# Performance work log

Measured on AMD Instinct MI355X. Metric: run time of the kernel, lower is better.

The kernel has to match this reference:

```python
import jax, jax.numpy as jnp
import numpy as np

D = 256       # hp.encoder_dim
F = 256       # hp.duration_predictor_filter_size
K = 3         # hp.duration_predictor_kernel_size
ALPHA = 1.0
EPS = 1e-5


def _conv1d(x, w):
    # x: [N, L, Cin], w: [K, Cin, Cout], 'same' padding=1 for K=3
    return jax.lax.conv_general_dilated(
        x, w, window_strides=(1,), padding=((1, 1),),
        dimension_numbers=('NWC', 'WIO', 'NWC'))


def _layer_norm(h, g, b):
    mu = jnp.mean(h, axis=-1, keepdims=True)
    var = jnp.var(h, axis=-1, keepdims=True)
    return (h - mu) * jax.lax.rsqrt(var + EPS) * g + b


def setup_inputs() -> dict:
    key = jax.random.key(0)
    ks = jax.random.split(key, 12)
    N, L = 16, 512
    xavier_cw = float(np.sqrt(2.0 / (D * K + F * K)))  # xavier-ish for conv
    xavier_lw = float(np.sqrt(2.0 / (F + 1)))
    return {
        'x': jax.random.normal(ks[0], (N, L, D), dtype=jnp.float32),
        'conv1_w': jax.random.normal(ks[1], (K, D, F), dtype=jnp.float32) * xavier_cw,
        'conv1_b': jnp.zeros((F,), dtype=jnp.float32),
        'ln1_g': jnp.ones((F,), dtype=jnp.float32),
        'ln1_b': jnp.zeros((F,), dtype=jnp.float32),
        'conv2_w': jax.random.normal(ks[2], (K, F, F), dtype=jnp.float32) * xavier_cw,
        'conv2_b': jnp.zeros((F,), dtype=jnp.float32),
        'ln2_g': jnp.ones((F,), dtype=jnp.float32),
        'ln2_b': jnp.zeros((F,), dtype=jnp.float32),
        'lin_w': jax.random.normal(ks[3], (F, 1), dtype=jnp.float32) * xavier_lw,
        'lin_b': jnp.zeros((1,), dtype=jnp.float32),
        'WVF_max_length': 4096,
    }


def reference(x, conv1_w, conv1_b, ln1_g, ln1_b, conv2_w, conv2_b,
              ln2_g, ln2_b, lin_w, lin_b, WVF_max_length):
    # ---- DurationPredictor (eval mode: dropout = identity) ----
    h = _conv1d(x, conv1_w) + conv1_b            # [N, L, F]
    h = jax.nn.relu(_layer_norm(h, ln1_g, ln1_b))
    h = _conv1d(h, conv2_w) + conv2_b
    h = jax.nn.relu(_layer_norm(h, ln2_g, ln2_b))
    dpo = jax.nn.relu(h @ lin_w + lin_b)[..., 0]  # [N, L]

    # ---- LengthRegulator (no attn): int durations, alignment @ x ----
    dur = ((dpo + 0.5) * ALPHA).astype(jnp.int32)  # [N, L]
    ends = jnp.cumsum(dur, axis=-1)                # inclusive cumsum
    starts = ends - dur                            # exclusive cumsum
    t = jnp.arange(WVF_max_length)                 # static output length
    # alignment[n, t, l] = 1 iff starts[n,l] <= t < ends[n,l]
    align = ((t[None, :, None] >= starts[:, None, :]) &
             (t[None, :, None] < ends[:, None, :])).astype(x.dtype)  # [N, T, L]
    out = jnp.einsum('ntl,nld->ntd', align, x)     # [N, T, D]

    WVF_pos = jnp.arange(1, WVF_max_length + 1, dtype=jnp.int64
                         if jax.config.jax_enable_x64 else jnp.int32)[None, :]
    return out, WVF_pos
```

## Files before the change

kernel.cpp:

```cpp
#include <hip/hip_runtime.h>
#include <hip/hip_fp8.h>
#include <math.h>

#define N_   16
#define L_   512
#define C_   256
#define T_   4096
#define EPSL 1e-5f
#define BM   32

typedef float f32x4 __attribute__((ext_vector_type(4)));

__device__ __forceinline__ unsigned char f2q(float f) {
    __hip_fp8_e4m3 q(f);
    return (unsigned char)q.__x;
}

__global__ __launch_bounds__(256) void pack_w_kernel(
    const float* __restrict__ w1, const float* __restrict__ w2,
    unsigned char* __restrict__ bpk1, unsigned char* __restrict__ bpk2,
    float* __restrict__ wpos)
{
    int gid = blockIdx.x * 256 + threadIdx.x;
    if (gid < T_) wpos[gid] = (float)(gid + 1);
    const float* w      = (gid < 24576) ? w1 : w2;
    unsigned char* bpk  = (gid < 24576) ? bpk1 : bpk2;
    int g2 = gid & 24575;
    int lane = g2 & 63;
    int s    = (g2 >> 6) & 7;
    int cg   = (g2 >> 9) & 15;
    int karm = g2 >> 13;
    int cin0 = s * 32 + (lane >> 4) * 8;
    int cout = cg * 16 + (lane & 15);
    const float* src = w + (size_t)(karm * 256 + cin0) * 256 + cout;
    unsigned long long o = 0;
    #pragma unroll
    for (int e = 0; e < 8; ++e)
        o |= (unsigned long long)f2q(src[(size_t)e * 256]) << (8 * e);
    *reinterpret_cast<unsigned long long*>(bpk + (size_t)g2 * 8) = o;
}

#define LDB(BPK, KARM, DST) do {                                              \
    const unsigned char* bb_ = (BPK) + ((size_t)((KARM) * 16 + cg0)) * 4096 + lane * 8; \
    _Pragma("unroll")                                                         \
    for (int s_ = 0; s_ < 8; ++s_) {                                          \
        DST[s_]     = *reinterpret_cast<const long*>(bb_ + s_ * 512);         \
        DST[8 + s_] = *reinterpret_cast<const long*>(bb_ + 4096 + s_ * 512);  \
    } } while (0)

#define AOFF(BUF, RA, S)                                                      \
    (BUF + (RA) * 256 + (((((S) << 1) + (lg >> 1)) ^ ((RA) & 15)) << 4) + ((lg & 1) << 3))

#define CONV1K(KARM, B) do {                                                  \
    _Pragma("unroll")                                                         \
    for (int s_ = 0; s_ < 8; ++s_) {                                          \
        _Pragma("unroll")                                                     \
        for (int t_ = 0; t_ < 3; ++t_) {                                      \
            int rA_ = 16 * t_ + lr + (KARM);                                  \
            long a_ = *reinterpret_cast<const long*>(AOFF(xt, rA_, s_));      \
            acc1[t_][0] = __builtin_amdgcn_mfma_f32_16x16x32_fp8_fp8(a_, B[s_],     acc1[t_][0], 0, 0, 0); \
            acc1[t_][1] = __builtin_amdgcn_mfma_f32_16x16x32_fp8_fp8(a_, B[8 + s_], acc1[t_][1], 0, 0, 0); \
        } } } while (0)

#define CONV2K(KARM, B) do {                                                  \
    _Pragma("unroll")                                                         \
    for (int s_ = 0; s_ < 8; ++s_) {                                          \
        _Pragma("unroll")                                                     \
        for (int t_ = 0; t_ < 2; ++t_) {                                      \
            int rA_ = 16 * t_ + lr + (KARM);                                  \
            long a_ = *reinterpret_cast<const long*>(AOFF(h1t, rA_, s_));     \
            c2[t_][0] = __builtin_amdgcn_mfma_f32_16x16x32_fp8_fp8(a_, B[s_],     c2[t_][0], 0, 0, 0); \
            c2[t_][1] = __builtin_amdgcn_mfma_f32_16x16x32_fp8_fp8(a_, B[8 + s_], c2[t_][1], 0, 0, 0); \
        } } } while (0)

__global__ __launch_bounds__(512) void fused_conv_kernel(
    const float* __restrict__ x,
    const unsigned char* __restrict__ bpk1, const unsigned char* __restrict__ bpk2,
    const float* __restrict__ b1, const float* __restrict__ g1, const float* __restrict__ be1,
    const float* __restrict__ b2, const float* __restrict__ g2, const float* __restrict__ be2,
    const float* __restrict__ lw, const float* __restrict__ lb,
    int* __restrict__ dur)
{
    __shared__ __align__(16) char xt[50 * 256];
    __shared__ __align__(16) char h1t[34 * 256];
    __shared__ float redS[8][48], redQ[8][48], redP[8][32];

    const int tid  = threadIdx.x;
    const int wv   = tid >> 6;
    const int lane = tid & 63;
    const int lg   = lane >> 4;
    const int lr   = lane & 15;
    const int n    = blockIdx.x >> 4;
    const int l0   = (blockIdx.x & 15) << 5;
    const int cg0  = wv * 2;
    const int col0 = wv * 32 + lr, col1 = col0 + 16;

    long Ba[16], Bb[16];
    LDB(bpk1, 0, Ba);

    for (int idx = tid; idx < 36 * 16; idx += 512) {
        int r = idx >> 4, slot = idx & 15;
        int l = l0 - 2 + r;
        unsigned int pk[4] = {0, 0, 0, 0};
        if (l >= 0 && l < L_) {
            const float* src = x + (((size_t)(n * L_ + l)) << 8) + (slot << 4);
            #pragma unroll
            for (int q = 0; q < 4; ++q) {
                f32x4 f = *reinterpret_cast<const f32x4*>(src + q * 4);
                pk[q] = (unsigned int)f2q(f[0]) | ((unsigned int)f2q(f[1]) << 8) |
                        ((unsigned int)f2q(f[2]) << 16) | ((unsigned int)f2q(f[3]) << 24);
            }
        }
        *reinterpret_cast<uint4*>(xt + r * 256 + ((slot ^ (r & 15)) << 4)) =
            make_uint4(pk[0], pk[1], pk[2], pk[3]);
    }
    __syncthreads();

    f32x4 acc1[3][2] = {};
    LDB(bpk1, 1, Bb);  CONV1K(0, Ba);
    LDB(bpk1, 2, Ba);  CONV1K(1, Bb);
    LDB(bpk2, 0, Bb);  CONV1K(2, Ba);
    LDB(bpk2, 1, Ba);

    const float cb10 = b1[col0], cb11 = b1[col1];
    const float cg10 = g1[col0], cg11 = g1[col1];
    const float ce10 = be1[col0], ce11 = be1[col1];
    {
        float sv[12], qv[12];
        #pragma unroll
        for (int t = 0; t < 3; ++t)
            #pragma unroll
            for (int j = 0; j < 4; ++j) {
                float h0 = acc1[t][0][j] + cb10, h1 = acc1[t][1][j] + cb11;
                sv[t*4+j] = h0 + h1; qv[t*4+j] = h0 * h0 + h1 * h1;
            }
        #pragma unroll
        for (int m = 1; m < 16; m <<= 1)
            #pragma unroll
            for (int k = 0; k < 12; ++k) {
                sv[k] += __shfl_xor(sv[k], m, 64);
                qv[k] += __shfl_xor(qv[k], m, 64);
            }
        if (lr == 0) {
            #pragma unroll
            for (int t = 0; t < 3; ++t)
                #pragma unroll
                for (int j = 0; j < 4; ++j) {
                    redS[wv][16*t + lg*4 + j] = sv[t*4+j];
                    redQ[wv][16*t + lg*4 + j] = qv[t*4+j];
                }
        }
    }
    __syncthreads();
    if (tid < 48) {
        float ss = 0.f, qq = 0.f;
        #pragma unroll
        for (int u = 0; u < 8; ++u) { ss += redS[u][tid]; qq += redQ[u][tid]; }
        float m_  = ss * (1.f / 256.f);
        float var = fmaxf(qq * (1.f / 256.f) - m_ * m_, 0.f);
        redS[0][tid] = m_;
        redQ[0][tid] = 1.0f / sqrtf(var + EPSL);
    }
    __syncthreads();

    #pragma unroll
    for (int t = 0; t < 3; ++t)
        #pragma unroll
        for (int j = 0; j < 4; ++j) {
            int hr = 16*t + lg*4 + j;
            if (hr < 34) {
                int hl = l0 - 1 + hr;
                float r0 = 0.f, r1 = 0.f;
                if (hl >= 0 && hl < L_) {
                    r0 = fmaxf((acc1[t][0][j] + cb10 - redS[0][hr]) * redQ[0][hr] * cg10 + ce10, 0.f);
                    r1 = fmaxf((acc1[t][1][j] + cb11 - redS[0][hr]) * redQ[0][hr] * cg11 + ce11, 0.f);
                }
                *(unsigned char*)(h1t + hr*256 + (((col0 >> 4) ^ (hr & 15)) << 4) + (col0 & 15)) = f2q(r0);
                *(unsigned char*)(h1t + hr*256 + (((col1 >> 4) ^ (hr & 15)) << 4) + (col1 & 15)) = f2q(r1);
            }
        }
    __syncthreads();

    f32x4 c2[2][2] = {};
    CONV2K(0, Bb);  LDB(bpk2, 2, Bb);
    CONV2K(1, Ba);
    CONV2K(2, Bb);

    const float cb20 = b2[col0], cb21 = b2[col1];
    const float cg20 = g2[col0], cg21 = g2[col1];
    const float ce20 = be2[col0], ce21 = be2[col1];
    const float lw0  = lw[col0],  lw1  = lw[col1];
    {
        float sv[8], qv[8];
        #pragma unroll
        for (int tt = 0; tt < 2; ++tt)
            #pragma unroll
            for (int j = 0; j < 4; ++j) {
                float h0 = c2[tt][0][j] + cb20, h1 = c2[tt][1][j] + cb21;
                sv[tt*4+j] = h0 + h1; qv[tt*4+j] = h0 * h0 + h1 * h1;
            }
        #pragma unroll
        for (int m = 1; m < 16; m <<= 1)
            #pragma unroll
            for (int k = 0; k < 8; ++k) {
                sv[k] += __shfl_xor(sv[k], m, 64);
                qv[k] += __shfl_xor(qv[k], m, 64);
            }
        if (lr == 0) {
            #pragma unroll
            for (int tt = 0; tt < 2; ++tt)
                #pragma unroll
                for (int j = 0; j < 4; ++j) {
                    redS[wv][16*tt + lg*4 + j] = sv[tt*4+j];
                    redQ[wv][16*tt + lg*4 + j] = qv[tt*4+j];
                }
        }
    }
    __syncthreads();
    if (tid < 32) {
        float ss = 0.f, qq = 0.f;
        #pragma unroll
        for (int u = 0; u < 8; ++u) { ss += redS[u][tid]; qq += redQ[u][tid]; }
        float m_  = ss * (1.f / 256.f);
        float var = fmaxf(qq * (1.f / 256.f) - m_ * m_, 0.f);
        redS[0][tid] = m_;
        redQ[0][tid] = 1.0f / sqrtf(var + EPSL);
    }
    __syncthreads();

    {
        float pv[8];
        #pragma unroll
        for (int tt = 0; tt < 2; ++tt)
            #pragma unroll
            for (int j = 0; j < 4; ++j) {
                int r = 16*tt + lg*4 + j;
                float r0 = fmaxf((c2[tt][0][j] + cb20 - redS[0][r]) * redQ[0][r] * cg20 + ce20, 0.f);
                float r1 = fmaxf((c2[tt][1][j] + cb21 - redS[0][r]) * redQ[0][r] * cg21 + ce21, 0.f);
                pv[tt*4+j] = r0 * lw0 + r1 * lw1;
            }
        #pragma unroll
        for (int m = 1; m < 16; m <<= 1)
            #pragma unroll
            for (int k = 0; k < 8; ++k)
                pv[k] += __shfl_xor(pv[k], m, 64);
        if (lr == 0) {
            #pragma unroll
            for (int tt = 0; tt < 2; ++tt)
                #pragma unroll
                for (int j = 0; j < 4; ++j)
                    redP[wv][16*tt + lg*4 + j] = pv[tt*4+j];
        }
    }
    __syncthreads();
    if (tid < 32) {
        float dot = lb[0];
        #pragma unroll
        for (int u = 0; u < 8; ++u) dot += redP[u][tid];
        dur[n * L_ + l0 + tid] = (int)(fmaxf(dot, 0.f) + 0.5f);
    }
}

__global__ __launch_bounds__(512) void gather_kernel(
    const float* __restrict__ x, const int* __restrict__ dur,
    float* __restrict__ out)
{
    __shared__ __align__(16) int se[L_];
    const int wid = threadIdx.x >> 6, lane = threadIdx.x & 63;
    const int blk = blockIdx.x;
    const int n = blk >> 9;

    if (wid == 0) {
        const int* dsrc = dur + n * L_;
        int4 va = reinterpret_cast<const int4*>(dsrc)[lane * 2];
        int4 vb = reinterpret_cast<const int4*>(dsrc)[lane * 2 + 1];
        int p0 = va.x,      p1 = p0 + va.y, p2 = p1 + va.z, p3 = p2 + va.w;
        int p4 = p3 + vb.x, p5 = p4 + vb.y, p6 = p5 + vb.z, p7 = p6 + vb.w;
        int tot = p7;
        #pragma unroll
        for (int m = 1; m < 64; m <<= 1) {
            int tu = __shfl_up(tot, m, 64);
            if (lane >= m) tot += tu;
        }
        int off = tot - p7;
        reinterpret_cast<int4*>(se)[lane * 2]     = make_int4(p0+off, p1+off, p2+off, p3+off);
        reinterpret_cast<int4*>(se)[lane * 2 + 1] = make_int4(p4+off, p5+off, p6+off, p7+off);
    }
    __syncthreads();

    const int t = ((blk & 511) << 3) + wid;
    const int total = se[L_ - 1];

    f32x4 v = {0.f, 0.f, 0.f, 0.f};
    if (t < total) {
        int p = 0;
        #pragma unroll
        for (int step = 256; step > 0; step >>= 1)
            if (p + step <= L_ && se[p + step - 1] <= t) p += step;
        v = reinterpret_cast<const f32x4*>(x + (((size_t)(n * L_ + p)) << 8))[lane];
    }
    __builtin_nontemporal_store(
        v, reinterpret_cast<f32x4*>(out + (((size_t)(n * T_ + t)) << 8)) + lane);
}

extern "C" void kernel_launch(void* const* d_in, const int* in_sizes, int n_in,
                              void* d_out, int out_size, void* d_ws, size_t ws_size,
                              hipStream_t stream)
{
    const float* x   = (const float*)d_in[0];
    const float* w1  = (const float*)d_in[1];
    const float* b1  = (const float*)d_in[2];
    const float* g1  = (const float*)d_in[3];
    const float* be1 = (const float*)d_in[4];
    const float* w2  = (const float*)d_in[5];
    const float* b2  = (const float*)d_in[6];
    const float* g2  = (const float*)d_in[7];
    const float* be2 = (const float*)d_in[8];
    const float* lw  = (const float*)d_in[9];
    const float* lb  = (const float*)d_in[10];

    float* out = (float*)d_out;
    unsigned char* bpk1 = (unsigned char*)d_out;
    unsigned char* bpk2 = bpk1 + 196608;
    int* dur = (int*)d_ws;

    pack_w_kernel<<<192, 256, 0, stream>>>(w1, w2, bpk1, bpk2,
                                           out + (size_t)N_ * T_ * C_);

    fused_conv_kernel<<<N_ * (L_ / BM), 512, 0, stream>>>(
        x, bpk1, bpk2, b1, g1, be1, b2, g2, be2, lw, lb, dur);

    gather_kernel<<<N_ * T_ / 8, 512, 0, stream>>>(x, dur, out);
}
```

Before: 37.25 us.

## Halve conv row tile to 16 and use 4 waves covering 64 channels each

The fused conv/layernorm kernel now processes 16 sequence rows per block with 256 threads instead of 32 rows with 512 threads, so it launches twice as many blocks. Each wave covers 64 output channels (four 16-wide column groups) and loads weights in two halves per kernel tap. The aim is to spread the small prologue kernel across more CUs and cut the halo overhead of the 3-tap convolutions (34→18 rows of conv1 output). The cost is that every block reloads all the weights and recomputes a larger halo relative to its tile.

```diff
diff --git a/kernel.cpp b/kernel.cpp
--- a/kernel.cpp
+++ b/kernel.cpp
@@ -7,7 +7,7 @@
 #define C_   256
 #define T_   4096
 #define EPSL 1e-5f
-#define BM   32
+#define BM   16
 
 typedef float f32x4 __attribute__((ext_vector_type(4)));
 
@@ -40,8 +40,9 @@
     *reinterpret_cast<unsigned long long*>(bpk + (size_t)g2 * 8) = o;
 }
 
-#define LDB(BPK, KARM, DST) do {                                              \
-    const unsigned char* bb_ = (BPK) + ((size_t)((KARM) * 16 + cg0)) * 4096 + lane * 8; \
+#define LDB(BPK, KARM, HOFF, DST) do {                                        \
+    const unsigned char* bb_ = (BPK) +                                        \
+        ((size_t)((KARM) * 16 + (wv << 2) + ((HOFF) << 1))) * 4096 + lane * 8;\
     _Pragma("unroll")                                                         \
     for (int s_ = 0; s_ < 8; ++s_) {                                          \
         DST[s_]     = *reinterpret_cast<const long*>(bb_ + s_ * 512);         \
@@ -51,29 +52,27 @@
 #define AOFF(BUF, RA, S)                                                      \
     (BUF + (RA) * 256 + (((((S) << 1) + (lg >> 1)) ^ ((RA) & 15)) << 4) + ((lg & 1) << 3))
 
-#define CONV1K(KARM, B) do {                                                  \
-    _Pragma("unroll")                                                         \
-    for (int s_ = 0; s_ < 8; ++s_) {                                          \
-        _Pragma("unroll")                                                     \
-        for (int t_ = 0; t_ < 3; ++t_) {                                      \
-            int rA_ = 16 * t_ + lr + (KARM);                                  \
-            long a_ = *reinterpret_cast<const long*>(AOFF(xt, rA_, s_));      \
-            acc1[t_][0] = __builtin_amdgcn_mfma_f32_16x16x32_fp8_fp8(a_, B[s_],     acc1[t_][0], 0, 0, 0); \
-            acc1[t_][1] = __builtin_amdgcn_mfma_f32_16x16x32_fp8_fp8(a_, B[8 + s_], acc1[t_][1], 0, 0, 0); \
-        } } } while (0)
-
-#define CONV2K(KARM, B) do {                                                  \
+#define C1K(KARM, HOFF, B) do {                                               \
     _Pragma("unroll")                                                         \
     for (int s_ = 0; s_ < 8; ++s_) {                                          \
         _Pragma("unroll")                                                     \
         for (int t_ = 0; t_ < 2; ++t_) {                                      \
             int rA_ = 16 * t_ + lr + (KARM);                                  \
-            long a_ = *reinterpret_cast<const long*>(AOFF(h1t, rA_, s_));     \
-            c2[t_][0] = __builtin_amdgcn_mfma_f32_16x16x32_fp8_fp8(a_, B[s_],     c2[t_][0], 0, 0, 0); \
-            c2[t_][1] = __builtin_amdgcn_mfma_f32_16x16x32_fp8_fp8(a_, B[8 + s_], c2[t_][1], 0, 0, 0); \
+            long a_ = *reinterpret_cast<const long*>(AOFF(xt, rA_, s_));      \
+            acc1[t_][(HOFF)*2]     = __builtin_amdgcn_mfma_f32_16x16x32_fp8_fp8(a_, B[s_],     acc1[t_][(HOFF)*2],     0, 0, 0); \
+            acc1[t_][(HOFF)*2 + 1] = __builtin_amdgcn_mfma_f32_16x16x32_fp8_fp8(a_, B[8 + s_], acc1[t_][(HOFF)*2 + 1], 0, 0, 0); \
         } } } while (0)
 
-__global__ __launch_bounds__(512) void fused_conv_kernel(
+#define C2K(KARM, HOFF, B) do {                                               \
+    _Pragma("unroll")                                                         \
+    for (int s_ = 0; s_ < 8; ++s_) {                                          \
+        int rA_ = lr + (KARM);                                                \
+        long a_ = *reinterpret_cast<const long*>(AOFF(h1t, rA_, s_));         \
+        c2[(HOFF)*2]     = __builtin_amdgcn_mfma_f32_16x16x32_fp8_fp8(a_, B[s_],     c2[(HOFF)*2],     0, 0, 0); \
+        c2[(HOFF)*2 + 1] = __builtin_amdgcn_mfma_f32_16x16x32_fp8_fp8(a_, B[8 + s_], c2[(HOFF)*2 + 1], 0, 0, 0); \
+    } } while (0)
+
+__global__ __launch_bounds__(256) void fused_conv_kernel(
     const float* __restrict__ x,
     const unsigned char* __restrict__ bpk1, const unsigned char* __restrict__ bpk2,
     const float* __restrict__ b1, const float* __restrict__ g1, const float* __restrict__ be1,
@@ -81,24 +80,22 @@
     const float* __restrict__ lw, const float* __restrict__ lb,
     int* __restrict__ dur)
 {
-    __shared__ __align__(16) char xt[50 * 256];
-    __shared__ __align__(16) char h1t[34 * 256];
-    __shared__ float redS[8][48], redQ[8][48], redP[8][32];
+    __shared__ __align__(16) char xt[34 * 256];
+    __shared__ __align__(16) char h1t[18 * 256];
+    __shared__ float redS[4][32], redQ[4][32], redP[4][16];
 
     const int tid  = threadIdx.x;
     const int wv   = tid >> 6;
     const int lane = tid & 63;
     const int lg   = lane >> 4;
     const int lr   = lane & 15;
-    const int n    = blockIdx.x >> 4;
-    const int l0   = (blockIdx.x & 15) << 5;
-    const int cg0  = wv * 2;
-    const int col0 = wv * 32 + lr, col1 = col0 + 16;
+    const int n    = blockIdx.x >> 5;
+    const int l0   = (blockIdx.x & 31) << 4;
 
     long Ba[16], Bb[16];
-    LDB(bpk1, 0, Ba);
-
-    for (int idx = tid; idx < 36 * 16; idx += 512) {
+    LDB(bpk1, 0, 0, Ba);
+
+    for (int idx = tid; idx < 20 * 16; idx += 256) {
         int r = idx >> 4, slot = idx & 15;
         int l = l0 - 2 + r;
         unsigned int pk[4] = {0, 0, 0, 0};
@@ -116,34 +113,47 @@
     }
     __syncthreads();
 
-    f32x4 acc1[3][2] = {};
-    LDB(bpk1, 1, Bb);  CONV1K(0, Ba);
-    LDB(bpk1, 2, Ba);  CONV1K(1, Bb);
-    LDB(bpk2, 0, Bb);  CONV1K(2, Ba);
-    LDB(bpk2, 1, Ba);
-
-    const float cb10 = b1[col0], cb11 = b1[col1];
-    const float cg10 = g1[col0], cg11 = g1[col1];
-    const float ce10 = be1[col0], ce11 = be1[col1];
+    f32x4 acc1[2][4] = {};
+    LDB(bpk1, 0, 1, Bb);  C1K(0, 0, Ba);
+    LDB(bpk1, 1, 0, Ba);  C1K(0, 1, Bb);
+    LDB(bpk1, 1, 1, Bb);  C1K(1, 0, Ba);
+    LDB(bpk1, 2, 0, Ba);  C1K(1, 1, Bb);
+    LDB(bpk1, 2, 1, Bb);  C1K(2, 0, Ba);
+    LDB(bpk2, 0, 0, Ba);  C1K(2, 1, Bb);
+    LDB(bpk2, 0, 1, Bb);
+
+    int col[4];
+    float cb1[4], cg1v[4], ce1v[4];
+    #pragma unroll
+    for (int c = 0; c < 4; ++c) {
+        col[c] = wv * 64 + c * 16 + lr;
+        cb1[c] = b1[col[c]]; cg1v[c] = g1[col[c]]; ce1v[c] = be1[col[c]];
+    }
+
     {
-        float sv[12], qv[12];
-        #pragma unroll
-        for (int t = 0; t < 3; ++t)
+        float sv[8], qv[8];
+        #pragma unroll
+        for (int t = 0; t < 2; ++t)
             #pragma unroll
             for (int j = 0; j < 4; ++j) {
-                float h0 = acc1[t][0][j] + cb10, h1 = acc1[t][1][j] + cb11;
-                sv[t*4+j] = h0 + h1; qv[t*4+j] = h0 * h0 + h1 * h1;
+                float s_ = 0.f, q_ = 0.f;
+                #pragma unroll
+                for (int c = 0; c < 4; ++c) {
+                    float h = acc1[t][c][j] + cb1[c];
+                    s_ += h; q_ += h * h;
+                }
+                sv[t*4+j] = s_; qv[t*4+j] = q_;
             }
         #pragma unroll
         for (int m = 1; m < 16; m <<= 1)
             #pragma unroll
-            for (int k = 0; k < 12; ++k) {
+            for (int k = 0; k < 8; ++k) {
                 sv[k] += __shfl_xor(sv[k], m, 64);
                 qv[k] += __shfl_xor(qv[k], m, 64);
             }
         if (lr == 0) {
             #pragma unroll
-            for (int t = 0; t < 3; ++t)
+            for (int t = 0; t < 2; ++t)
                 #pragma unroll
                 for (int j = 0; j < 4; ++j) {
                     redS[wv][16*t + lg*4 + j] = sv[t*4+j];
@@ -152,10 +162,9 @@
         }
     }
     __syncthreads();
-    if (tid < 48) {
-        float ss = 0.f, qq = 0.f;
-        #pragma unroll
-        for (int u = 0; u < 8; ++u) { ss += redS[u][tid]; qq += redQ[u][tid]; }
+    if (tid < 32) {
+        float ss = redS[0][tid] + redS[1][tid] + redS[2][tid] + redS[3][tid];
+        float qq = redQ[0][tid] + redQ[1][tid] + redQ[2][tid] + redQ[3][tid];
         float m_  = ss * (1.f / 256.f);
         float var = fmaxf(qq * (1.f / 256.f) - m_ * m_, 0.f);
         redS[0][tid] = m_;
@@ -164,63 +173,68 @@
     __syncthreads();
 
     #pragma unroll
-    for (int t = 0; t < 3; ++t)
+    for (int t = 0; t < 2; ++t)
         #pragma unroll
         for (int j = 0; j < 4; ++j) {
             int hr = 16*t + lg*4 + j;
-            if (hr < 34) {
+            if (hr < 18) {
                 int hl = l0 - 1 + hr;
-                float r0 = 0.f, r1 = 0.f;
-                if (hl >= 0 && hl < L_) {
-                    r0 = fmaxf((acc1[t][0][j] + cb10 - redS[0][hr]) * redQ[0][hr] * cg10 + ce10, 0.f);
-                    r1 = fmaxf((acc1[t][1][j] + cb11 - redS[0][hr]) * redQ[0][hr] * cg11 + ce11, 0.f);
+                float mean = redS[0][hr], rstd = redQ[0][hr];
+                #pragma unroll
+                for (int c = 0; c < 4; ++c) {
+                    float r = 0.f;
+                    if (hl >= 0 && hl < L_)
+                        r = fmaxf((acc1[t][c][j] + cb1[c] - mean) * rstd * cg1v[c] + ce1v[c], 0.f);
+                    *(unsigned char*)(h1t + hr*256 + (((col[c] >> 4) ^ (hr & 15)) << 4) + (col[c] & 15)) = f2q(r);
                 }
-                *(unsigned char*)(h1t + hr*256 + (((col0 >> 4) ^ (hr & 15)) << 4) + (col0 & 15)) = f2q(r0);
-                *(unsigned char*)(h1t + hr*256 + (((col1 >> 4) ^ (hr & 15)) << 4) + (col1 & 15)) = f2q(r1);
-            }
-        }
-    __syncthreads();
-
-    f32x4 c2[2][2] = {};
-    CONV2K(0, Bb);  LDB(bpk2, 2, Bb);
-    CONV2K(1, Ba);
-    CONV2K(2, Bb);
-
-    const float cb20 = b2[col0], cb21 = b2[col1];
-    const float cg20 = g2[col0], cg21 = g2[col1];
-    const float ce20 = be2[col0], ce21 = be2[col1];
-    const float lw0  = lw[col0],  lw1  = lw[col1];
+            }
+        }
+    __syncthreads();
+
+    f32x4 c2[4] = {};
+    C2K(0, 0, Ba);  LDB(bpk2, 1, 0, Ba);
+    C2K(0, 1, Bb);  LDB(bpk2, 1, 1, Bb);
+    C2K(1, 0, Ba);  LDB(bpk2, 2, 0, Ba);
+    C2K(1, 1, Bb);  LDB(bpk2, 2, 1, Bb);
+    C2K(2, 0, Ba);
+    C2K(2, 1, Bb);
+
+    float cb2[4], cg2v[4], ce2v[4], lwv[4];
+    #pragma unroll
+    for (int c = 0; c < 4; ++c) {
+        cb2[c] = b2[col[c]]; cg2v[c] = g2[col[c]]; ce2v[c] = be2[col[c]]; lwv[c] = lw[col[c]];
+    }
     {
-        float sv[8], qv[8];
-        #pragma unroll
-        for (int tt = 0; tt < 2; ++tt)
-            #pragma unroll
-            for (int j = 0; j < 4; ++j) {
-                float h0 = c2[tt][0][j] + cb20, h1 = c2[tt][1][j] + cb21;
-                sv[tt*4+j] = h0 + h1; qv[tt*4+j] = h0 * h0 + h1 * h1;
-            }
+        float sv[4], qv[4];
+        #pragma unroll
+        for (int j = 0; j < 4; ++j) {
+            float s_ = 0.f, q_ = 0.f;
+            #pragma unroll
+            for (int c = 0; c < 4; ++c) {
+                float h = c2[c][j] + cb2[c];
+                s_ += h; q_ += h * h;
+            }
+            sv[j] = s_; qv[j] = q_;
+        }
         #pragma unroll
         for (int m = 1; m < 16; m <<= 1)
             #pragma unroll
-            for (int k = 0; k < 8; ++k) {
+            for (int k = 0; k < 4; ++k) {
                 sv[k] += __shfl_xor(sv[k], m, 64);
                 qv[k] += __shfl_xor(qv[k], m, 64);
             }
         if (lr == 0) {
             #pragma unroll
-            for (int tt = 0; tt < 2; ++tt)
-                #pragma unroll
-                for (int j = 0; j < 4; ++j) {
-                    redS[wv][16*tt + lg*4 + j] = sv[tt*4+j];
-                    redQ[wv][16*tt + lg*4 + j] = qv[tt*4+j];
-                }
-        }
-    }
-    __syncthreads();
-    if (tid < 32) {
-        float ss = 0.f, qq = 0.f;
-        #pragma unroll
-        for (int u = 0; u < 8; ++u) { ss += redS[u][tid]; qq += redQ[u][tid]; }
+            for (int j = 0; j < 4; ++j) {
+                redS[wv][lg*4 + j] = sv[j];
+                redQ[wv][lg*4 + j] = qv[j];
+            }
+        }
+    }
+    __syncthreads();
+    if (tid < 16) {
+        float ss = redS[0][tid] + redS[1][tid] + redS[2][tid] + redS[3][tid];
+        float qq = redQ[0][tid] + redQ[1][tid] + redQ[2][tid] + redQ[3][tid];
         float m_  = ss * (1.f / 256.f);
         float var = fmaxf(qq * (1.f / 256.f) - m_ * m_, 0.f);
         redS[0][tid] = m_;
@@ -229,34 +243,32 @@
     __syncthreads();
 
     {
-        float pv[8];
-        #pragma unroll
-        for (int tt = 0; tt < 2; ++tt)
-            #pragma unroll
-            for (int j = 0; j < 4; ++j) {
-                int r = 16*tt + lg*4 + j;
-                float r0 = fmaxf((c2[tt][0][j] + cb20 - redS[0][r]) * redQ[0][r] * cg20 + ce20, 0.f);
-                float r1 = fmaxf((c2[tt][1][j] + cb21 - redS[0][r]) * redQ[0][r] * cg21 + ce21, 0.f);
-                pv[tt*4+j] = r0 * lw0 + r1 * lw1;
-            }
+        float pv[4];
+        #pragma unroll
+        for (int j = 0; j < 4; ++j) {
+            int r = lg*4 + j;
+            float mean = redS[0][r], rstd = redQ[0][r];
+            float p_ = 0.f;
+            #pragma unroll
+            for (int c = 0; c < 4; ++c) {
+                float rl = fmaxf((c2[c][j] + cb2[c] - mean) * rstd * cg2v[c] + ce2v[c], 0.f);
+                p_ += rl * lwv[c];
+            }
+            pv[j] = p_;
+        }
         #pragma unroll
         for (int m = 1; m < 16; m <<= 1)
             #pragma unroll
-            for (int k = 0; k < 8; ++k)
+            for (int k = 0; k < 4; ++k)
                 pv[k] += __shfl_xor(pv[k], m, 64);
         if (lr == 0) {
             #pragma unroll
-            for (int tt = 0; tt < 2; ++tt)
-                #pragma unroll
-                for (int j = 0; j < 4; ++j)
-                    redP[wv][16*tt + lg*4 + j] = pv[tt*4+j];
-        }
-    }
-    __syncthreads();
-    if (tid < 32) {
-        float dot = lb[0];
-        #pragma unroll
-        for (int u = 0; u < 8; ++u) dot += redP[u][tid];
+            for (int j = 0; j < 4; ++j) redP[wv][lg*4 + j] = pv[j];
+        }
+    }
+    __syncthreads();
+    if (tid < 16) {
+        float dot = lb[0] + redP[0][tid] + redP[1][tid] + redP[2][tid] + redP[3][tid];
         dur[n * L_ + l0 + tid] = (int)(fmaxf(dot, 0.f) + 0.5f);
     }
 }
@@ -327,7 +339,7 @@
     pack_w_kernel<<<192, 256, 0, stream>>>(w1, w2, bpk1, bpk2,
                                            out + (size_t)N_ * T_ * C_);
 
-    fused_conv_kernel<<<N_ * (L_ / BM), 512, 0, stream>>>(
+    fused_conv_kernel<<<N_ * (L_ / BM), 256, 0, stream>>>(
         x, bpk1, bpk2, b1, g1, be1, b2, g2, be2, lw, lb, dur);
 
     gather_kernel<<<N_ * T_ / 8, 512, 0, stream>>>(x, dur, out);
```

After: 39.55 us (median of 2 runs). 1.06x slower.

## Repack fp8 weights for 16-byte loads and triple-buffer weight registers

Applied to the files above, without the earlier changes.

The weight packing kernel now places two consecutive k-slices per lane next to each other, so the conv kernel can fetch B fragments with 16-byte vector loads instead of 8-byte loads. A third register buffer is added so every weight slab is prefetched earlier: conv2's final slab is loaded before the LayerNorm stage instead of between conv2 MFMA groups. This is meant to hide global load latency behind compute, at the cost of 16 more 64-bit registers per thread, which may reduce occupancy. The pack kernel is launched with half as many blocks, each thread packing two words.

```diff
diff --git a/kernel.cpp b/kernel.cpp
--- a/kernel.cpp
+++ b/kernel.cpp
@@ -10,6 +10,7 @@
 #define BM   32
 
 typedef float f32x4 __attribute__((ext_vector_type(4)));
+typedef long  long2v __attribute__((ext_vector_type(2)));
 
 __device__ __forceinline__ unsigned char f2q(float f) {
     __hip_fp8_e4m3 q(f);
@@ -23,29 +24,36 @@
 {
     int gid = blockIdx.x * 256 + threadIdx.x;
     if (gid < T_) wpos[gid] = (float)(gid + 1);
-    const float* w      = (gid < 24576) ? w1 : w2;
-    unsigned char* bpk  = (gid < 24576) ? bpk1 : bpk2;
-    int g2 = gid & 24575;
+    const float* w      = (gid < 12288) ? w1 : w2;
+    unsigned char* bpk  = (gid < 12288) ? bpk1 : bpk2;
+    int g2 = gid & 12287;
     int lane = g2 & 63;
-    int s    = (g2 >> 6) & 7;
-    int cg   = (g2 >> 9) & 15;
-    int karm = g2 >> 13;
-    int cin0 = s * 32 + (lane >> 4) * 8;
+    int fp   = (g2 >> 6) & 3;
+    int cg   = (g2 >> 8) & 15;
+    int karm = g2 >> 12;
     int cout = cg * 16 + (lane & 15);
-    const float* src = w + (size_t)(karm * 256 + cin0) * 256 + cout;
-    unsigned long long o = 0;
+    int cin0 = (2 * fp) * 32 + (lane >> 4) * 8;
+    const float* s0 = w + (size_t)(karm * 256 + cin0) * 256 + cout;
+    const float* s1 = s0 + (size_t)32 * 256;
+    unsigned long long o0 = 0, o1 = 0;
     #pragma unroll
-    for (int e = 0; e < 8; ++e)
-        o |= (unsigned long long)f2q(src[(size_t)e * 256]) << (8 * e);
-    *reinterpret_cast<unsigned long long*>(bpk + (size_t)g2 * 8) = o;
+    for (int e = 0; e < 8; ++e) {
+        o0 |= (unsigned long long)f2q(s0[(size_t)e * 256]) << (8 * e);
+        o1 |= (unsigned long long)f2q(s1[(size_t)e * 256]) << (8 * e);
+    }
+    unsigned long long* dst =
+        reinterpret_cast<unsigned long long*>(bpk + (size_t)g2 * 16);
+    dst[0] = o0; dst[1] = o1;
 }
 
 #define LDB(BPK, KARM, DST) do {                                              \
-    const unsigned char* bb_ = (BPK) + ((size_t)((KARM) * 16 + cg0)) * 4096 + lane * 8; \
+    const unsigned char* bb_ = (BPK) + ((size_t)((KARM) * 16 + cg0)) * 4096 + lane * 16; \
     _Pragma("unroll")                                                         \
-    for (int s_ = 0; s_ < 8; ++s_) {                                          \
-        DST[s_]     = *reinterpret_cast<const long*>(bb_ + s_ * 512);         \
-        DST[8 + s_] = *reinterpret_cast<const long*>(bb_ + 4096 + s_ * 512);  \
+    for (int f_ = 0; f_ < 4; ++f_) {                                          \
+        long2v v0_ = *reinterpret_cast<const long2v*>(bb_ + f_ * 1024);       \
+        long2v v1_ = *reinterpret_cast<const long2v*>(bb_ + 4096 + f_ * 1024);\
+        DST[2*f_]     = v0_[0];  DST[2*f_ + 1]     = v0_[1];                  \
+        DST[8 + 2*f_] = v1_[0];  DST[8 + 2*f_ + 1] = v1_[1];                  \
     } } while (0)
 
 #define AOFF(BUF, RA, S)                                                      \
@@ -95,8 +103,9 @@
     const int cg0  = wv * 2;
     const int col0 = wv * 32 + lr, col1 = col0 + 16;
 
-    long Ba[16], Bb[16];
+    long Ba[16], Bb[16], Bc[16];
     LDB(bpk1, 0, Ba);
+    LDB(bpk1, 1, Bb);
 
     for (int idx = tid; idx < 36 * 16; idx += 512) {
         int r = idx >> 4, slot = idx & 15;
@@ -117,10 +126,10 @@
     __syncthreads();
 
     f32x4 acc1[3][2] = {};
-    LDB(bpk1, 1, Bb);  CONV1K(0, Ba);
-    LDB(bpk1, 2, Ba);  CONV1K(1, Bb);
-    LDB(bpk2, 0, Bb);  CONV1K(2, Ba);
-    LDB(bpk2, 1, Ba);
+    LDB(bpk1, 2, Bc);  CONV1K(0, Ba);
+    LDB(bpk2, 0, Ba);  CONV1K(1, Bb);
+    LDB(bpk2, 1, Bb);  CONV1K(2, Bc);
+    LDB(bpk2, 2, Bc);
 
     const float cb10 = b1[col0], cb11 = b1[col1];
     const float cg10 = g1[col0], cg11 = g1[col1];
@@ -182,9 +191,9 @@
     __syncthreads();
 
     f32x4 c2[2][2] = {};
-    CONV2K(0, Bb);  LDB(bpk2, 2, Bb);
-    CONV2K(1, Ba);
-    CONV2K(2, Bb);
+    CONV2K(0, Ba);
+    CONV2K(1, Bb);
+    CONV2K(2, Bc);
 
     const float cb20 = b2[col0], cb21 = b2[col1];
     const float cg20 = g2[col0], cg21 = g2[col1];
@@ -324,8 +333,8 @@
     unsigned char* bpk2 = bpk1 + 196608;
     int* dur = (int*)d_ws;
 
-    pack_w_kernel<<<192, 256, 0, stream>>>(w1, w2, bpk1, bpk2,
-                                           out + (size_t)N_ * T_ * C_);
+    pack_w_kernel<<<96, 256, 0, stream>>>(w1, w2, bpk1, bpk2,
+                                          out + (size_t)N_ * T_ * C_);
 
     fused_conv_kernel<<<N_ * (L_ / BM), 512, 0, stream>>>(
         x, bpk1, bpk2, b1, g1, be1, b2, g2, be2, lw, lb, dur);
```

Measured after the change: 36.89 us. No clear change (-1.0%).
